# Kernel optimization log

Hardware: AMD Instinct MI355X
Metric: run time of the kernel (lower is better)

## Reference

```python
import jax, jax.numpy as jnp
import numpy as np

B, N, M, E, H = 8, 4096, 4, 512, 8
HEAD_DIM = E // H
LN_EPS = 1e-5


def setup_inputs() -> dict:
    key = jax.random.key(0)
    ks = jax.random.split(key, 12)
    inp = {}
    for i in range(M):
        inp[f"f{i}"] = jax.random.normal(ks[i], (B, N, E), dtype=jnp.float32)
    # learned query (flattened from [1,1,E])
    inp["q_param"] = jax.random.normal(ks[4], (E,), dtype=jnp.float32)
    # torch nn.MultiheadAttention packed in-projection [3E, E] and bias [3E]
    inp["in_proj_w"] = jax.random.normal(ks[5], (3 * E, E), dtype=jnp.float32) * 0.02
    inp["in_proj_b"] = jnp.zeros((3 * E,), dtype=jnp.float32)
    inp["out_proj_w"] = jax.random.normal(ks[6], (E, E), dtype=jnp.float32) * 0.02
    inp["out_proj_b"] = jnp.zeros((E,), dtype=jnp.float32)
    inp["ln_gamma"] = jnp.ones((E,), dtype=jnp.float32)
    inp["ln_beta"] = jnp.zeros((E,), dtype=jnp.float32)
    return inp


def reference(f0, f1, f2, f3, q_param, in_proj_w, in_proj_b, out_proj_w, out_proj_b, ln_gamma, ln_beta):
    x = jnp.stack([f0, f1, f2, f3], axis=2)  # [B, N, M, E]
    b, n, m, e = x.shape
    h, d = H, e // H
    scale = 1.0 / np.sqrt(d)

    Wq, Wk, Wv = jnp.split(in_proj_w, 3, axis=0)  # each [E, E]
    bq, bk, bv = jnp.split(in_proj_b, 3)

    # single learned query, shared across all (b, n) instances
    qh = ((Wq @ q_param + bq) * scale).reshape(h, d)  # [H, d]

    k = (jnp.einsum('bnme,fe->bnmf', x, Wk) + bk).reshape(b, n, m, h, d)
    v = (jnp.einsum('bnme,fe->bnmf', x, Wv) + bv).reshape(b, n, m, h, d)

    scores = jnp.einsum('hd,bnmhd->bnhm', qh, k)        # [B, N, H, M]
    attn = jax.nn.softmax(scores, axis=-1)
    o = jnp.einsum('bnhm,bnmhd->bnhd', attn, v).reshape(b, n, e)
    o = o @ out_proj_w.T + out_proj_b                   # [B, N, E]

    mu = jnp.mean(o, axis=-1, keepdims=True)
    var = jnp.var(o, axis=-1, keepdims=True)
    return (o - mu) * jax.lax.rsqrt(var + LN_EPS) * ln_gamma + ln_beta
```

## Files before the change

### kernel.cpp

```cpp
#include <hip/hip_runtime.h>
#include <hip/hip_bf16.h>


typedef float  f32x4  __attribute__((ext_vector_type(4)));
typedef float  f32x16 __attribute__((ext_vector_type(16)));
typedef short  short8 __attribute__((ext_vector_type(8)));

__device__ __forceinline__ unsigned short f2bf(float f) {
  unsigned int x = __float_as_uint(f);
  unsigned int r = (x + 0x7fffu + ((x >> 16) & 1u)) >> 16;
  return (unsigned short)r;
}

__device__ __forceinline__ short8 pack8(const f32x4& a, const f32x4& b) {
  short8 r;
  r[0] = (short)f2bf(a[0]); r[1] = (short)f2bf(a[1]);
  r[2] = (short)f2bf(a[2]); r[3] = (short)f2bf(a[3]);
  r[4] = (short)f2bf(b[0]); r[5] = (short)f2bf(b[1]);
  r[6] = (short)f2bf(b[2]); r[7] = (short)f2bf(b[3]);
  return r;
}

__device__ __forceinline__ void mfma32(f32x16& c, short8 a, short8 b) {
  asm("v_mfma_f32_32x32x16_bf16 %0, %1, %2, %0" : "+v"(c) : "v"(a), "v"(b));
}
__device__ __forceinline__ void mfma16(f32x4& c, short8 a, short8 b) {
  asm("v_mfma_f32_16x16x32_bf16 %0, %1, %2, %0" : "+v"(c) : "v"(a), "v"(b));
}

__device__ __forceinline__ void gld4f(f32x4& d, const float* p) {
  asm volatile("global_load_dwordx4 %0, %1, off" : "=v"(d) : "v"(p));
}
__device__ __forceinline__ void gld4s(short8& d, const unsigned short* p) {
  asm volatile("global_load_dwordx4 %0, %1, off" : "=v"(d) : "v"(p));
}

__device__ __forceinline__ void wxv4(f32x4& a, f32x4& b, f32x4& c, f32x4& d) {
  asm volatile("s_waitcnt vmcnt(4)" : "+v"(a), "+v"(b), "+v"(c), "+v"(d));
}
__device__ __forceinline__ void wxv8(f32x4& a, f32x4& b, f32x4& c, f32x4& d) {
  asm volatile("s_waitcnt vmcnt(8)" : "+v"(a), "+v"(b), "+v"(c), "+v"(d));
}
__device__ __forceinline__ void wxv12(f32x4& a, f32x4& b, f32x4& c, f32x4& d) {
  asm volatile("s_waitcnt vmcnt(12)" : "+v"(a), "+v"(b), "+v"(c), "+v"(d));
}
__device__ __forceinline__ void wbv4(short8& a, short8& b, short8& c, short8& d,
                                     short8& e, short8& f, short8& g, short8& h) {
  asm volatile("s_waitcnt vmcnt(4)"
               : "+v"(a), "+v"(b), "+v"(c), "+v"(d),
                 "+v"(e), "+v"(f), "+v"(g), "+v"(h));
}
__device__ __forceinline__ void wbv0(short8& a, short8& b, short8& c, short8& d,
                                     short8& e, short8& f, short8& g, short8& h) {
  asm volatile("s_waitcnt vmcnt(0)"
               : "+v"(a), "+v"(b), "+v"(c), "+v"(d),
                 "+v"(e), "+v"(f), "+v"(g), "+v"(h));
}

__global__ void __launch_bounds__(512) tdcp_k0(
    const float* __restrict__ q_param, const float* __restrict__ in_w,
    const float* __restrict__ in_b, const float* __restrict__ out_w,
    float* __restrict__ scoreb, unsigned short* __restrict__ wscB,
    unsigned short* __restrict__ WvB, unsigned short* __restrict__ WoB)
{
  const int tid = threadIdx.x;
  const int blk = blockIdx.x;
  if (blk < 8) {
    const int h = blk;
    __shared__ float qls[512];
    __shared__ float qs[64];
    qls[tid] = q_param[tid];
    __syncthreads();
    {
      const int io = tid >> 3, sub = tid & 7;
      const float* wrow = in_w + (size_t)(h * 64 + io) * 512;
      float v = 0.f;
      #pragma unroll 8
      for (int ee = 0; ee < 64; ++ee) {
        const int e = sub + (ee << 3);
        v += wrow[e] * qls[e];
      }
      v += __shfl_xor(v, 1); v += __shfl_xor(v, 2); v += __shfl_xor(v, 4);
      if (sub == 0) qs[io] = (v + in_b[h * 64 + io]) * 0.125f;
    }
    __syncthreads();
    {
      const int e = tid;
      const float* wk = in_w + (size_t)(512 + h * 64) * 512 + e;
      float v = 0.f;
      #pragma unroll 8
      for (int jj = 0; jj < 64; ++jj) v += qs[jj] * wk[jj * 512];
      const int s32 = e >> 5, g = (e & 31) >> 3, j = e & 7;
      wscB[((s32 << 6) + h + (g << 4)) * 8 + j] = f2bf(v);
      wscB[((s32 << 6) + (h + 8) + (g << 4)) * 8 + j] = 0;
    }
    if (tid < 64) {
      float v = qs[tid] * in_b[512 + h * 64 + tid];
      v += __shfl_xor(v, 1);  v += __shfl_xor(v, 2);  v += __shfl_xor(v, 4);
      v += __shfl_xor(v, 8);  v += __shfl_xor(v, 16); v += __shfl_xor(v, 32);
      if (tid == 0) scoreb[h] = v;
    }
    if (blk == 0 && tid >= 64 && tid < 72) scoreb[tid - 56] = 0.f;
  } else {
    const int mb = blk - 8;
    const bool isWo = mb >= 64;
    const float* src = isWo ? out_w : (in_w + (size_t)1024 * 512);
    unsigned short* dst = isWo ? WoB : WvB;
    const int slot = ((mb & 63) << 9) + tid;
    const int ct = slot >> 11, kt = (slot >> 6) & 31, ln = slot & 63;
    const float* p = src + (size_t)(ct * 32 + (ln & 31)) * 512
                         + kt * 16 + ((ln >> 5) << 3);
    const f32x4 u0 = *(const f32x4*)(p);
    const f32x4 u1 = *(const f32x4*)(p + 4);
    *(short8*)(dst + slot * 8) = pack8(u0, u1);
  }
}

__global__ void __launch_bounds__(512, 2) tdcp_k1(
    const float* __restrict__ f0, const float* __restrict__ f1,
    const float* __restrict__ f2, const float* __restrict__ f3,
    const float* __restrict__ in_b,
    const float* __restrict__ scoreb, const unsigned short* __restrict__ wscB,
    const unsigned short* __restrict__ WvB, const unsigned short* __restrict__ WoB,
    const float* __restrict__ out_b, const float* __restrict__ gamma,
    const float* __restrict__ beta, float* __restrict__ out)
{
  __shared__ __align__(16) char smem[65536];
  const int tid = threadIdx.x;
  const int w = tid >> 6;
  const int l = tid & 63;
  const int tok0 = blockIdx.x << 5;

  {
    const f32x4* wsrc = (const f32x4*)wscB;
    f32x4* wdst = (f32x4*)(smem + 49152);
    wdst[tid * 2] = wsrc[tid * 2];
    wdst[tid * 2 + 1] = wsrc[tid * 2 + 1];
  }

  const int sr = tid >> 2;
  const int chunk = tid & 3;
  const int sm = sr & 3;
  const int stk = sr >> 2;
  const float* fsrc = (sm == 0 ? f0 : sm == 1 ? f1 : sm == 2 ? f2 : f3)
                      + (size_t)(tok0 + stk) * 512 + (chunk << 4);
  const int wbase = (chunk << 12) + ((sr >> 5) << 10)
                  + (((sr & 31) << 4) ^ (chunk << 5));

  const int aO = ((l >> 5) << 9) + ((l & 31) << 4);
  const int sBase = ((w >> 1) << 10) + (((l >> 4) & 1) << 9)
                  + ((((w & 1) << 4) | (l & 15)) << 4);
  const int ct0 = w << 1;
  const unsigned short* wv0 = WvB + (((ct0 * 32) << 6) + l) * 8;
  const unsigned short* wv1 = WvB + ((((ct0 + 1) * 32) << 6) + l) * 8;
  const unsigned short* wscL = (const unsigned short*)(smem + 49152);

  f32x16 acc[4][2];
  f32x4 sacc;
  #pragma unroll
  for (int i = 0; i < 4; ++i)
    #pragma unroll
    for (int c = 0; c < 2; ++c)
      #pragma unroll
      for (int r = 0; r < 16; ++r) acc[i][c][r] = 0.f;
  sacc[0] = sacc[1] = sacc[2] = sacc[3] = 0.f;

  f32x4 lx[2][4];
  short8 bb[2][8];

  gld4f(lx[0][0], fsrc);      gld4f(lx[0][1], fsrc + 4);
  gld4f(lx[0][2], fsrc + 8);  gld4f(lx[0][3], fsrc + 12);
  gld4f(lx[1][0], fsrc + 64); gld4f(lx[1][1], fsrc + 68);
  gld4f(lx[1][2], fsrc + 72); gld4f(lx[1][3], fsrc + 76);
  wxv4(lx[0][0], lx[0][1], lx[0][2], lx[0][3]);
  *(short8*)(smem + wbase) = pack8(lx[0][0], lx[0][1]);
  *(short8*)(smem + wbase + 512) = pack8(lx[0][2], lx[0][3]);
  #pragma unroll
  for (int j = 0; j < 4; ++j) {
    gld4s(bb[0][2 * j],     wv0 + j * 512);
    gld4s(bb[0][2 * j + 1], wv1 + j * 512);
  }
  gld4f(lx[0][0], fsrc + 128); gld4f(lx[0][1], fsrc + 132);
  gld4f(lx[0][2], fsrc + 136); gld4f(lx[0][3], fsrc + 140);
  asm volatile("s_waitcnt lgkmcnt(0)" ::: "memory");
  __builtin_amdgcn_s_barrier();
  asm volatile("" ::: "memory");

  #pragma unroll
  for (int s = 0; s < 8; ++s) {
    if (s < 7) {
      f32x4 (&L)[4] = lx[(s + 1) & 1];
      if (s < 6) wxv12(L[0], L[1], L[2], L[3]);
      else       wxv8(L[0], L[1], L[2], L[3]);
      char* nb = smem + 16384 * ((s + 1) % 3);
      *(short8*)(nb + wbase) = pack8(L[0], L[1]);
      *(short8*)(nb + wbase + 512) = pack8(L[2], L[3]);
    }
    asm volatile("s_waitcnt lgkmcnt(0)" ::: "memory");
    __builtin_amdgcn_s_barrier();
    asm volatile("" ::: "memory");

    short8 (&b)[8] = bb[s & 1];
    if (s < 6) wbv4(b[0], b[1], b[2], b[3], b[4], b[5], b[6], b[7]);
    else       wbv0(b[0], b[1], b[2], b[3], b[4], b[5], b[6], b[7]);
    char* cur = smem + 16384 * (s % 3);
    const short8 sb0 = *(const short8*)(wscL + (((2 * s) << 6) + l) * 8);
    const short8 sb1 = *(const short8*)(wscL + (((2 * s + 1) << 6) + l) * 8);
    #pragma unroll
    for (int kt4 = 0; kt4 < 4; ++kt4) {
      #pragma unroll
      for (int rt = 0; rt < 4; ++rt) {
        const short8 a = *(const short8*)(cur + (kt4 << 12) + (rt << 10)
                                          + (aO ^ (kt4 << 5)));
        mfma32(acc[rt][0], a, b[kt4 * 2]);
        mfma32(acc[rt][1], a, b[kt4 * 2 + 1]);
      }
      if ((kt4 & 1) == 0) {
        const int schunk = kt4 + (l >> 5);
        const short8 sa = *(const short8*)(cur + (schunk << 12)
                                           + (sBase ^ ((schunk & 3) << 5)));
        mfma16(sacc, sa, (kt4 == 0) ? sb0 : sb1);
      }
    }
    if (s < 7) {
      short8 (&nbf)[8] = bb[(s + 1) & 1];
      #pragma unroll
      for (int j = 0; j < 4; ++j) {
        gld4s(nbf[2 * j],     wv0 + ((s + 1) * 4 + j) * 512);
        gld4s(nbf[2 * j + 1], wv1 + ((s + 1) * 4 + j) * 512);
      }
    }
    if (s < 5) {
      f32x4 (&L)[4] = lx[(s + 3) & 1];
      const float* p = fsrc + ((s + 3) << 6);
      gld4f(L[0], p); gld4f(L[1], p + 4); gld4f(L[2], p + 8); gld4f(L[3], p + 12);
    }
  }
  asm volatile("s_nop 7\n\ts_nop 7\n\ts_nop 7" ::);

  {
    const int hh = l & 15;
    if (hh < 8) {
      const float sb = scoreb[hh];
      const float s0 = sacc[0] + sb, s1 = sacc[1] + sb;
      const float s2 = sacc[2] + sb, s3 = sacc[3] + sb;
      const float mx = fmaxf(fmaxf(s0, s1), fmaxf(s2, s3));
      const float e0 = __expf(s0 - mx), e1 = __expf(s1 - mx);
      const float e2 = __expf(s2 - mx), e3 = __expf(s3 - mx);
      const float inv = 1.f / (e0 + e1 + e2 + e3);
      f32x4 av; av[0] = e0 * inv; av[1] = e1 * inv; av[2] = e2 * inv; av[3] = e3 * inv;
      const int t = (w << 2) + (l >> 4);
      *(f32x4*)(smem + 32768 + (((t << 3) + hh) << 4)) = av;
    }
  }
  __syncthreads();

  {
    unsigned short* omid = (unsigned short*)(smem);
    #pragma unroll
    for (int c2 = 0; c2 < 2; ++c2) {
      const int ff = ((ct0 + c2) << 5) + (l & 31);
      const float bvf = in_b[1024 + ff];
      const int ktf = ff >> 4;
      const int laneL = ((l >> 3) & 1) << 5;
      const int elem = ff & 7;
      #pragma unroll
      for (int rt = 0; rt < 4; ++rt) {
        #pragma unroll
        for (int tt = 0; tt < 4; ++tt) {
          const int t = (rt << 3) + (tt << 1) + (l >> 5);
          const f32x4 av = *(const f32x4*)(smem + 32768 + (((t << 3) + w) << 4));
          const float o = av[0] * acc[rt][c2][tt * 4 + 0]
                        + av[1] * acc[rt][c2][tt * 4 + 1]
                        + av[2] * acc[rt][c2][tt * 4 + 2]
                        + av[3] * acc[rt][c2][tt * 4 + 3] + bvf;
          omid[((ktf << 6) + t + laneL) * 8 + elem] = f2bf(o);
        }
      }
    }
  }
  __syncthreads();

  f32x16 oa0, oa1;
  #pragma unroll
  for (int r = 0; r < 16; ++r) { oa0[r] = 0.f; oa1[r] = 0.f; }
  const int a_off = l << 4;
  #pragma unroll 4
  for (int kt = 0; kt < 32; ++kt) {
    const short8 a = *(const short8*)(smem + (kt << 10) + a_off);
    const short8 b0 = *(const short8*)(WoB + (((ct0 * 32 + kt) << 6) + l) * 8);
    const short8 b1 = *(const short8*)(WoB + ((((ct0 + 1) * 32 + kt) << 6) + l) * 8);
    mfma32(oa0, a, b0);
    mfma32(oa1, a, b1);
  }
  asm volatile("s_nop 7\n\ts_nop 7\n\ts_nop 7" ::);

  {
    const int g0 = (ct0 << 5) + (l & 31);
    const int g1 = g0 + 32;
    const float ob0 = out_b[g0], ob1 = out_b[g1];
    const float gm0 = gamma[g0], gm1 = gamma[g1];
    const float bt0 = beta[g0],  bt1 = beta[g1];
    float* stats = (float*)(smem + 36864);
    #pragma unroll
    for (int r = 0; r < 16; ++r) {
      const float v0 = oa0[r] + ob0, v1 = oa1[r] + ob1;
      float s = v0 + v1, qq = v0 * v0 + v1 * v1;
      s += __shfl_xor(s, 16); qq += __shfl_xor(qq, 16);
      s += __shfl_xor(s, 8);  qq += __shfl_xor(qq, 8);
      s += __shfl_xor(s, 4);  qq += __shfl_xor(qq, 4);
      s += __shfl_xor(s, 2);  qq += __shfl_xor(qq, 2);
      s += __shfl_xor(s, 1);  qq += __shfl_xor(qq, 1);
      if ((l & 31) == 0) {
        const int t = (r & 3) + ((r >> 2) << 3) + ((l >> 5) << 2);
        stats[(t << 4) + (w << 1)] = s;
        stats[(t << 4) + (w << 1) + 1] = qq;
      }
    }
    __syncthreads();
    #pragma unroll
    for (int r = 0; r < 16; ++r) {
      const int t = (r & 3) + ((r >> 2) << 3) + ((l >> 5) << 2);
      const float* st = stats + (t << 4);
      float s = 0.f, qq = 0.f;
      #pragma unroll
      for (int ww = 0; ww < 8; ++ww) { s += st[2 * ww]; qq += st[2 * ww + 1]; }
      const float mu = s * 0.001953125f;
      const float rs = rsqrtf(qq * 0.001953125f - mu * mu + 1e-5f);
      const float v0 = oa0[r] + ob0, v1 = oa1[r] + ob1;
      float* op = out + (size_t)(tok0 + t) * 512;
      op[g0] = (v0 - mu) * rs * gm0 + bt0;
      op[g1] = (v1 - mu) * rs * gm1 + bt1;
    }
  }
}

extern "C" void kernel_launch(void* const* d_in, const int* in_sizes, int n_in,
                              void* d_out, int out_size, void* d_ws, size_t ws_size,
                              hipStream_t stream) {
  const float* f0      = (const float*)d_in[0];
  const float* f1      = (const float*)d_in[1];
  const float* f2      = (const float*)d_in[2];
  const float* f3      = (const float*)d_in[3];
  const float* q_param = (const float*)d_in[4];
  const float* in_w    = (const float*)d_in[5];
  const float* in_b    = (const float*)d_in[6];
  const float* out_w   = (const float*)d_in[7];
  const float* out_b   = (const float*)d_in[8];
  const float* gamma   = (const float*)d_in[9];
  const float* beta    = (const float*)d_in[10];
  float* out = (float*)d_out;

  char* ws = (char*)d_ws;
  float* scoreb          = (float*)ws;
  unsigned short* wscB   = (unsigned short*)(ws + 4096);
  unsigned short* WvB    = (unsigned short*)(ws + 20480);
  unsigned short* WoB    = (unsigned short*)(ws + 544768);

  tdcp_k0<<<136, 512, 0, stream>>>(q_param, in_w, in_b, out_w,
                                   scoreb, wscB, WvB, WoB);
  tdcp_k1<<<1024, 512, 0, stream>>>(f0, f1, f2, f3, in_b,
                                    scoreb, wscB, WvB, WoB,
                                    out_b, gamma, beta, out);
}
```

Before: 152.6 us.

## Double block size to 16 waves, one output column tile per wave

The fused attention/out-projection kernel now runs 1024 threads per block instead of 512. Each wave owns a single 32-column tile of the V projection and of the output projection instead of two, which halves its accumulators, prefetched weight fragments and staged input registers. Staging loads, waitcnt depths and the LayerNorm statistics layout are resized to fit 16 waves, and only the first 8 waves compute the attention scores. Separately, bf16 packing now uses the hardware v_cvt_pk_bf16_f32 instruction instead of software rounding. The aim is to hide memory latency with more waves in flight; the risk is that the aggressive launch bounds squeeze registers too hard, and barriers across 16 waves cost more.

```diff
diff --git a/kernel.cpp b/kernel.cpp
--- a/kernel.cpp
+++ b/kernel.cpp
@@ -13,11 +13,16 @@
 }
 
 __device__ __forceinline__ short8 pack8(const f32x4& a, const f32x4& b) {
+  unsigned int r0, r1, r2, r3;
+  asm("v_cvt_pk_bf16_f32 %0, %1, %2" : "=v"(r0) : "v"(a[0]), "v"(a[1]));
+  asm("v_cvt_pk_bf16_f32 %0, %1, %2" : "=v"(r1) : "v"(a[2]), "v"(a[3]));
+  asm("v_cvt_pk_bf16_f32 %0, %1, %2" : "=v"(r2) : "v"(b[0]), "v"(b[1]));
+  asm("v_cvt_pk_bf16_f32 %0, %1, %2" : "=v"(r3) : "v"(b[2]), "v"(b[3]));
   short8 r;
-  r[0] = (short)f2bf(a[0]); r[1] = (short)f2bf(a[1]);
-  r[2] = (short)f2bf(a[2]); r[3] = (short)f2bf(a[3]);
-  r[4] = (short)f2bf(b[0]); r[5] = (short)f2bf(b[1]);
-  r[6] = (short)f2bf(b[2]); r[7] = (short)f2bf(b[3]);
+  r[0] = (short)(r0 & 0xffff); r[1] = (short)(r0 >> 16);
+  r[2] = (short)(r1 & 0xffff); r[3] = (short)(r1 >> 16);
+  r[4] = (short)(r2 & 0xffff); r[5] = (short)(r2 >> 16);
+  r[6] = (short)(r3 & 0xffff); r[7] = (short)(r3 >> 16);
   return r;
 }
 
@@ -35,26 +40,20 @@
   asm volatile("global_load_dwordx4 %0, %1, off" : "=v"(d) : "v"(p));
 }
 
-__device__ __forceinline__ void wxv4(f32x4& a, f32x4& b, f32x4& c, f32x4& d) {
-  asm volatile("s_waitcnt vmcnt(4)" : "+v"(a), "+v"(b), "+v"(c), "+v"(d));
-}
-__device__ __forceinline__ void wxv8(f32x4& a, f32x4& b, f32x4& c, f32x4& d) {
-  asm volatile("s_waitcnt vmcnt(8)" : "+v"(a), "+v"(b), "+v"(c), "+v"(d));
-}
-__device__ __forceinline__ void wxv12(f32x4& a, f32x4& b, f32x4& c, f32x4& d) {
-  asm volatile("s_waitcnt vmcnt(12)" : "+v"(a), "+v"(b), "+v"(c), "+v"(d));
-}
-__device__ __forceinline__ void wbv4(short8& a, short8& b, short8& c, short8& d,
-                                     short8& e, short8& f, short8& g, short8& h) {
-  asm volatile("s_waitcnt vmcnt(4)"
-               : "+v"(a), "+v"(b), "+v"(c), "+v"(d),
-                 "+v"(e), "+v"(f), "+v"(g), "+v"(h));
-}
-__device__ __forceinline__ void wbv0(short8& a, short8& b, short8& c, short8& d,
-                                     short8& e, short8& f, short8& g, short8& h) {
-  asm volatile("s_waitcnt vmcnt(0)"
-               : "+v"(a), "+v"(b), "+v"(c), "+v"(d),
-                 "+v"(e), "+v"(f), "+v"(g), "+v"(h));
+__device__ __forceinline__ void wxv2(f32x4& a, f32x4& b) {
+  asm volatile("s_waitcnt vmcnt(2)" : "+v"(a), "+v"(b));
+}
+__device__ __forceinline__ void wxv4(f32x4& a, f32x4& b) {
+  asm volatile("s_waitcnt vmcnt(4)" : "+v"(a), "+v"(b));
+}
+__device__ __forceinline__ void wxv6(f32x4& a, f32x4& b) {
+  asm volatile("s_waitcnt vmcnt(6)" : "+v"(a), "+v"(b));
+}
+__device__ __forceinline__ void wbv2(short8& a, short8& b, short8& c, short8& d) {
+  asm volatile("s_waitcnt vmcnt(2)" : "+v"(a), "+v"(b), "+v"(c), "+v"(d));
+}
+__device__ __forceinline__ void wbv0(short8& a, short8& b, short8& c, short8& d) {
+  asm volatile("s_waitcnt vmcnt(0)" : "+v"(a), "+v"(b), "+v"(c), "+v"(d));
 }
 
 __global__ void __launch_bounds__(512) tdcp_k0(
@@ -112,11 +111,18 @@
                          + kt * 16 + ((ln >> 5) << 3);
     const f32x4 u0 = *(const f32x4*)(p);
     const f32x4 u1 = *(const f32x4*)(p + 4);
-    *(short8*)(dst + slot * 8) = pack8(u0, u1);
-  }
-}
-
-__global__ void __launch_bounds__(512, 2) tdcp_k1(
+    unsigned int r0, r1, r2, r3;
+    short8 rr;
+    rr[0] = (short)f2bf(u0[0]); rr[1] = (short)f2bf(u0[1]);
+    rr[2] = (short)f2bf(u0[2]); rr[3] = (short)f2bf(u0[3]);
+    rr[4] = (short)f2bf(u1[0]); rr[5] = (short)f2bf(u1[1]);
+    rr[6] = (short)f2bf(u1[2]); rr[7] = (short)f2bf(u1[3]);
+    *(short8*)(dst + slot * 8) = rr;
+    (void)r0; (void)r1; (void)r2; (void)r3;
+  }
+}
+
+__global__ void __launch_bounds__(1024, 4) tdcp_k1(
     const float* __restrict__ f0, const float* __restrict__ f1,
     const float* __restrict__ f2, const float* __restrict__ f3,
     const float* __restrict__ in_b,
@@ -134,54 +140,44 @@
   {
     const f32x4* wsrc = (const f32x4*)wscB;
     f32x4* wdst = (f32x4*)(smem + 49152);
-    wdst[tid * 2] = wsrc[tid * 2];
-    wdst[tid * 2 + 1] = wsrc[tid * 2 + 1];
-  }
-
-  const int sr = tid >> 2;
-  const int chunk = tid & 3;
+    wdst[tid] = wsrc[tid];
+  }
+
+  const int sr = tid >> 3;
+  const int c16 = (tid & 7) >> 1;
+  const int half = tid & 1;
   const int sm = sr & 3;
   const int stk = sr >> 2;
   const float* fsrc = (sm == 0 ? f0 : sm == 1 ? f1 : sm == 2 ? f2 : f3)
-                      + (size_t)(tok0 + stk) * 512 + (chunk << 4);
-  const int wbase = (chunk << 12) + ((sr >> 5) << 10)
-                  + (((sr & 31) << 4) ^ (chunk << 5));
+                      + (size_t)(tok0 + stk) * 512 + ((tid & 7) << 3);
+  const int wbase = (c16 << 12) + ((sr >> 5) << 10)
+                  + (((sr & 31) << 4) ^ (c16 << 5)) + (half << 9);
 
   const int aO = ((l >> 5) << 9) + ((l & 31) << 4);
   const int sBase = ((w >> 1) << 10) + (((l >> 4) & 1) << 9)
                   + ((((w & 1) << 4) | (l & 15)) << 4);
-  const int ct0 = w << 1;
-  const unsigned short* wv0 = WvB + (((ct0 * 32) << 6) + l) * 8;
-  const unsigned short* wv1 = WvB + ((((ct0 + 1) * 32) << 6) + l) * 8;
+  const unsigned short* wv = WvB + (((w * 32) << 6) + l) * 8;
+  const unsigned short* wo = WoB + (((w * 32) << 6) + l) * 8;
   const unsigned short* wscL = (const unsigned short*)(smem + 49152);
 
-  f32x16 acc[4][2];
+  f32x16 acc[4];
   f32x4 sacc;
   #pragma unroll
   for (int i = 0; i < 4; ++i)
     #pragma unroll
-    for (int c = 0; c < 2; ++c)
-      #pragma unroll
-      for (int r = 0; r < 16; ++r) acc[i][c][r] = 0.f;
+    for (int r = 0; r < 16; ++r) acc[i][r] = 0.f;
   sacc[0] = sacc[1] = sacc[2] = sacc[3] = 0.f;
 
-  f32x4 lx[2][4];
-  short8 bb[2][8];
+  f32x4 lx[2][2];
+  short8 bb[4];
 
   gld4f(lx[0][0], fsrc);      gld4f(lx[0][1], fsrc + 4);
-  gld4f(lx[0][2], fsrc + 8);  gld4f(lx[0][3], fsrc + 12);
   gld4f(lx[1][0], fsrc + 64); gld4f(lx[1][1], fsrc + 68);
-  gld4f(lx[1][2], fsrc + 72); gld4f(lx[1][3], fsrc + 76);
-  wxv4(lx[0][0], lx[0][1], lx[0][2], lx[0][3]);
+  wxv2(lx[0][0], lx[0][1]);
   *(short8*)(smem + wbase) = pack8(lx[0][0], lx[0][1]);
-  *(short8*)(smem + wbase + 512) = pack8(lx[0][2], lx[0][3]);
   #pragma unroll
-  for (int j = 0; j < 4; ++j) {
-    gld4s(bb[0][2 * j],     wv0 + j * 512);
-    gld4s(bb[0][2 * j + 1], wv1 + j * 512);
-  }
+  for (int j = 0; j < 4; ++j) gld4s(bb[j], wv + j * 512);
   gld4f(lx[0][0], fsrc + 128); gld4f(lx[0][1], fsrc + 132);
-  gld4f(lx[0][2], fsrc + 136); gld4f(lx[0][3], fsrc + 140);
   asm volatile("s_waitcnt lgkmcnt(0)" ::: "memory");
   __builtin_amdgcn_s_barrier();
   asm volatile("" ::: "memory");
@@ -189,56 +185,50 @@
   #pragma unroll
   for (int s = 0; s < 8; ++s) {
     if (s < 7) {
-      f32x4 (&L)[4] = lx[(s + 1) & 1];
-      if (s < 6) wxv12(L[0], L[1], L[2], L[3]);
-      else       wxv8(L[0], L[1], L[2], L[3]);
+      f32x4 (&L)[2] = lx[(s + 1) & 1];
+      if (s < 6) wxv6(L[0], L[1]);
+      else       wxv4(L[0], L[1]);
       char* nb = smem + 16384 * ((s + 1) % 3);
       *(short8*)(nb + wbase) = pack8(L[0], L[1]);
-      *(short8*)(nb + wbase + 512) = pack8(L[2], L[3]);
     }
     asm volatile("s_waitcnt lgkmcnt(0)" ::: "memory");
     __builtin_amdgcn_s_barrier();
     asm volatile("" ::: "memory");
 
-    short8 (&b)[8] = bb[s & 1];
-    if (s < 6) wbv4(b[0], b[1], b[2], b[3], b[4], b[5], b[6], b[7]);
-    else       wbv0(b[0], b[1], b[2], b[3], b[4], b[5], b[6], b[7]);
+    if (s < 6) wbv2(bb[0], bb[1], bb[2], bb[3]);
+    else       wbv0(bb[0], bb[1], bb[2], bb[3]);
     char* cur = smem + 16384 * (s % 3);
-    const short8 sb0 = *(const short8*)(wscL + (((2 * s) << 6) + l) * 8);
-    const short8 sb1 = *(const short8*)(wscL + (((2 * s + 1) << 6) + l) * 8);
     #pragma unroll
     for (int kt4 = 0; kt4 < 4; ++kt4) {
       #pragma unroll
       for (int rt = 0; rt < 4; ++rt) {
         const short8 a = *(const short8*)(cur + (kt4 << 12) + (rt << 10)
                                           + (aO ^ (kt4 << 5)));
-        mfma32(acc[rt][0], a, b[kt4 * 2]);
-        mfma32(acc[rt][1], a, b[kt4 * 2 + 1]);
-      }
-      if ((kt4 & 1) == 0) {
+        mfma32(acc[rt], a, bb[kt4]);
+      }
+      if (w < 8 && (kt4 & 1) == 0) {
         const int schunk = kt4 + (l >> 5);
         const short8 sa = *(const short8*)(cur + (schunk << 12)
                                            + (sBase ^ ((schunk & 3) << 5)));
-        mfma16(sacc, sa, (kt4 == 0) ? sb0 : sb1);
+        const short8 sb = *(const short8*)(wscL
+                            + (((2 * s + (kt4 >> 1)) << 6) + l) * 8);
+        mfma16(sacc, sa, sb);
       }
     }
     if (s < 7) {
-      short8 (&nbf)[8] = bb[(s + 1) & 1];
       #pragma unroll
-      for (int j = 0; j < 4; ++j) {
-        gld4s(nbf[2 * j],     wv0 + ((s + 1) * 4 + j) * 512);
-        gld4s(nbf[2 * j + 1], wv1 + ((s + 1) * 4 + j) * 512);
-      }
+      for (int j = 0; j < 4; ++j)
+        gld4s(bb[j], wv + ((s + 1) * 4 + j) * 512);
     }
     if (s < 5) {
-      f32x4 (&L)[4] = lx[(s + 3) & 1];
+      f32x4 (&L)[2] = lx[(s + 3) & 1];
       const float* p = fsrc + ((s + 3) << 6);
-      gld4f(L[0], p); gld4f(L[1], p + 4); gld4f(L[2], p + 8); gld4f(L[3], p + 12);
+      gld4f(L[0], p); gld4f(L[1], p + 4);
     }
   }
   asm volatile("s_nop 7\n\ts_nop 7\n\ts_nop 7" ::);
 
-  {
+  if (w < 8) {
     const int hh = l & 15;
     if (hh < 8) {
       const float sb = scoreb[hh];
@@ -257,55 +247,50 @@
 
   {
     unsigned short* omid = (unsigned short*)(smem);
-    #pragma unroll
-    for (int c2 = 0; c2 < 2; ++c2) {
-      const int ff = ((ct0 + c2) << 5) + (l & 31);
-      const float bvf = in_b[1024 + ff];
-      const int ktf = ff >> 4;
-      const int laneL = ((l >> 3) & 1) << 5;
-      const int elem = ff & 7;
+    const int ff = (w << 5) + (l & 31);
+    const float bvf = in_b[1024 + ff];
+    const int ktf = ff >> 4;
+    const int laneL = ((l >> 3) & 1) << 5;
+    const int elem = ff & 7;
+    const int hq = w >> 1;
+    #pragma unroll
+    for (int rt = 0; rt < 4; ++rt) {
       #pragma unroll
-      for (int rt = 0; rt < 4; ++rt) {
-        #pragma unroll
-        for (int tt = 0; tt < 4; ++tt) {
-          const int t = (rt << 3) + (tt << 1) + (l >> 5);
-          const f32x4 av = *(const f32x4*)(smem + 32768 + (((t << 3) + w) << 4));
-          const float o = av[0] * acc[rt][c2][tt * 4 + 0]
-                        + av[1] * acc[rt][c2][tt * 4 + 1]
-                        + av[2] * acc[rt][c2][tt * 4 + 2]
-                        + av[3] * acc[rt][c2][tt * 4 + 3] + bvf;
-          omid[((ktf << 6) + t + laneL) * 8 + elem] = f2bf(o);
-        }
+      for (int tt = 0; tt < 4; ++tt) {
+        const int t = (rt << 3) + (tt << 1) + (l >> 5);
+        const f32x4 av = *(const f32x4*)(smem + 32768 + (((t << 3) + hq) << 4));
+        const float o = av[0] * acc[rt][tt * 4 + 0]
+                      + av[1] * acc[rt][tt * 4 + 1]
+                      + av[2] * acc[rt][tt * 4 + 2]
+                      + av[3] * acc[rt][tt * 4 + 3] + bvf;
+        omid[((ktf << 6) + t + laneL) * 8 + elem] = f2bf(o);
       }
     }
   }
   __syncthreads();
 
-  f32x16 oa0, oa1;
+  f32x16 oa;
   #pragma unroll
-  for (int r = 0; r < 16; ++r) { oa0[r] = 0.f; oa1[r] = 0.f; }
+  for (int r = 0; r < 16; ++r) oa[r] = 0.f;
   const int a_off = l << 4;
   #pragma unroll 4
   for (int kt = 0; kt < 32; ++kt) {
     const short8 a = *(const short8*)(smem + (kt << 10) + a_off);
-    const short8 b0 = *(const short8*)(WoB + (((ct0 * 32 + kt) << 6) + l) * 8);
-    const short8 b1 = *(const short8*)(WoB + ((((ct0 + 1) * 32 + kt) << 6) + l) * 8);
-    mfma32(oa0, a, b0);
-    mfma32(oa1, a, b1);
+    const short8 b0 = *(const short8*)(wo + kt * 512);
+    mfma32(oa, a, b0);
   }
   asm volatile("s_nop 7\n\ts_nop 7\n\ts_nop 7" ::);
 
   {
-    const int g0 = (ct0 << 5) + (l & 31);
-    const int g1 = g0 + 32;
-    const float ob0 = out_b[g0], ob1 = out_b[g1];
-    const float gm0 = gamma[g0], gm1 = gamma[g1];
-    const float bt0 = beta[g0],  bt1 = beta[g1];
+    const int g0 = (w << 5) + (l & 31);
+    const float ob0 = out_b[g0];
+    const float gm0 = gamma[g0];
+    const float bt0 = beta[g0];
     float* stats = (float*)(smem + 36864);
     #pragma unroll
     for (int r = 0; r < 16; ++r) {
-      const float v0 = oa0[r] + ob0, v1 = oa1[r] + ob1;
-      float s = v0 + v1, qq = v0 * v0 + v1 * v1;
+      const float v0 = oa[r] + ob0;
+      float s = v0, qq = v0 * v0;
       s += __shfl_xor(s, 16); qq += __shfl_xor(qq, 16);
       s += __shfl_xor(s, 8);  qq += __shfl_xor(qq, 8);
       s += __shfl_xor(s, 4);  qq += __shfl_xor(qq, 4);
@@ -313,24 +298,25 @@
       s += __shfl_xor(s, 1);  qq += __shfl_xor(qq, 1);
       if ((l & 31) == 0) {
         const int t = (r & 3) + ((r >> 2) << 3) + ((l >> 5) << 2);
-        stats[(t << 4) + (w << 1)] = s;
-        stats[(t << 4) + (w << 1) + 1] = qq;
+        stats[(t << 5) + (w << 1)] = s;
+        stats[(t << 5) + (w << 1) + 1] = qq;
       }
     }
     __syncthreads();
     #pragma unroll
     for (int r = 0; r < 16; ++r) {
       const int t = (r & 3) + ((r >> 2) << 3) + ((l >> 5) << 2);
-      const float* st = stats + (t << 4);
+      const float* st = (const float*)(smem + 36864) + (t << 5);
       float s = 0.f, qq = 0.f;
       #pragma unroll
-      for (int ww = 0; ww < 8; ++ww) { s += st[2 * ww]; qq += st[2 * ww + 1]; }
+      for (int ww = 0; ww < 8; ++ww) {
+        const f32x4 u = *(const f32x4*)(st + (ww << 2));
+        s += u[0] + u[2]; qq += u[1] + u[3];
+      }
       const float mu = s * 0.001953125f;
       const float rs = rsqrtf(qq * 0.001953125f - mu * mu + 1e-5f);
-      const float v0 = oa0[r] + ob0, v1 = oa1[r] + ob1;
-      float* op = out + (size_t)(tok0 + t) * 512;
-      op[g0] = (v0 - mu) * rs * gm0 + bt0;
-      op[g1] = (v1 - mu) * rs * gm1 + bt1;
+      const float v0 = oa[r] + ob0;
+      out[(size_t)(tok0 + t) * 512 + g0] = (v0 - mu) * rs * gm0 + bt0;
     }
   }
 }
@@ -359,7 +345,7 @@
 
   tdcp_k0<<<136, 512, 0, stream>>>(q_param, in_w, in_b, out_w,
                                    scoreb, wscB, WvB, WoB);
-  tdcp_k1<<<1024, 512, 0, stream>>>(f0, f1, f2, f3, in_b,
-                                    scoreb, wscB, WvB, WoB,
-                                    out_b, gamma, beta, out);
-}
+  tdcp_k1<<<1024, 1024, 0, stream>>>(f0, f1, f2, f3, in_b,
+                                     scoreb, wscB, WvB, WoB,
+                                     out_b, gamma, beta, out);
+}
```

Result: slower. 170.7 us (+11.8%).

## Use hardware bf16 pack conversion and interleave x-tile loads to strided 4-float chunks

Applied to the files above, without the earlier changes.

Replaces the software round-to-nearest bf16 conversion in the hot activation path with the v_cvt_pk_bf16_f32 instruction, keeping the software path only in the weight prep kernel. Changes how each thread loads its x slice, from 16 contiguous floats to four 4-float chunks strided by 16, and writes them as four 8-byte LDS stores at recomputed swizzled offsets. This aims to cut VALU conversion cost and improve global load coalescing across lanes. Also hoists the Wo pointer arithmetic out of the output GEMM loop. The new LDS layout must match the MFMA read pattern exactly, and the narrower stores could raise LDS store count or bank conflicts.

```diff
diff --git a/kernel.cpp b/kernel.cpp
--- a/kernel.cpp
+++ b/kernel.cpp
@@ -5,6 +5,7 @@
 typedef float  f32x4  __attribute__((ext_vector_type(4)));
 typedef float  f32x16 __attribute__((ext_vector_type(16)));
 typedef short  short8 __attribute__((ext_vector_type(8)));
+typedef unsigned int u32x2 __attribute__((ext_vector_type(2)));
 
 __device__ __forceinline__ unsigned short f2bf(float f) {
   unsigned int x = __float_as_uint(f);
@@ -13,11 +14,23 @@
 }
 
 __device__ __forceinline__ short8 pack8(const f32x4& a, const f32x4& b) {
+  unsigned int r0, r1, r2, r3;
+  asm("v_cvt_pk_bf16_f32 %0, %1, %2" : "=v"(r0) : "v"(a[0]), "v"(a[1]));
+  asm("v_cvt_pk_bf16_f32 %0, %1, %2" : "=v"(r1) : "v"(a[2]), "v"(a[3]));
+  asm("v_cvt_pk_bf16_f32 %0, %1, %2" : "=v"(r2) : "v"(b[0]), "v"(b[1]));
+  asm("v_cvt_pk_bf16_f32 %0, %1, %2" : "=v"(r3) : "v"(b[2]), "v"(b[3]));
   short8 r;
-  r[0] = (short)f2bf(a[0]); r[1] = (short)f2bf(a[1]);
-  r[2] = (short)f2bf(a[2]); r[3] = (short)f2bf(a[3]);
-  r[4] = (short)f2bf(b[0]); r[5] = (short)f2bf(b[1]);
-  r[6] = (short)f2bf(b[2]); r[7] = (short)f2bf(b[3]);
+  r[0] = (short)(r0 & 0xffff); r[1] = (short)(r0 >> 16);
+  r[2] = (short)(r1 & 0xffff); r[3] = (short)(r1 >> 16);
+  r[4] = (short)(r2 & 0xffff); r[5] = (short)(r2 >> 16);
+  r[6] = (short)(r3 & 0xffff); r[7] = (short)(r3 >> 16);
+  return r;
+}
+
+__device__ __forceinline__ u32x2 pack4(const f32x4& a) {
+  u32x2 r;
+  asm("v_cvt_pk_bf16_f32 %0, %1, %2" : "=v"(r[0]) : "v"(a[0]), "v"(a[1]));
+  asm("v_cvt_pk_bf16_f32 %0, %1, %2" : "=v"(r[1]) : "v"(a[2]), "v"(a[3]));
   return r;
 }
 
@@ -112,7 +125,12 @@
                          + kt * 16 + ((ln >> 5) << 3);
     const f32x4 u0 = *(const f32x4*)(p);
     const f32x4 u1 = *(const f32x4*)(p + 4);
-    *(short8*)(dst + slot * 8) = pack8(u0, u1);
+    short8 rr;
+    rr[0] = (short)f2bf(u0[0]); rr[1] = (short)f2bf(u0[1]);
+    rr[2] = (short)f2bf(u0[2]); rr[3] = (short)f2bf(u0[3]);
+    rr[4] = (short)f2bf(u1[0]); rr[5] = (short)f2bf(u1[1]);
+    rr[6] = (short)f2bf(u1[2]); rr[7] = (short)f2bf(u1[3]);
+    *(short8*)(dst + slot * 8) = rr;
   }
 }
 
@@ -139,13 +157,16 @@
   }
 
   const int sr = tid >> 2;
-  const int chunk = tid & 3;
+  const int c = tid & 3;
   const int sm = sr & 3;
   const int stk = sr >> 2;
   const float* fsrc = (sm == 0 ? f0 : sm == 1 ? f1 : sm == 2 ? f2 : f3)
-                      + (size_t)(tok0 + stk) * 512 + (chunk << 4);
-  const int wbase = (chunk << 12) + ((sr >> 5) << 10)
-                  + (((sr & 31) << 4) ^ (chunk << 5));
+                      + (size_t)(tok0 + stk) * 512 + (c << 2);
+  int wj[4];
+  #pragma unroll
+  for (int j = 0; j < 4; ++j)
+    wj[j] = (j << 12) + ((sr >> 5) << 10) + ((c >> 1) << 9)
+          + ((((sr & 31) << 4)) ^ (j << 5)) + ((c & 1) << 3);
 
   const int aO = ((l >> 5) << 9) + ((l & 31) << 4);
   const int sBase = ((w >> 1) << 10) + (((l >> 4) & 1) << 9)
@@ -160,28 +181,29 @@
   #pragma unroll
   for (int i = 0; i < 4; ++i)
     #pragma unroll
-    for (int c = 0; c < 2; ++c)
-      #pragma unroll
-      for (int r = 0; r < 16; ++r) acc[i][c][r] = 0.f;
+    for (int cc = 0; cc < 2; ++cc)
+      #pragma unroll
+      for (int r = 0; r < 16; ++r) acc[i][cc][r] = 0.f;
   sacc[0] = sacc[1] = sacc[2] = sacc[3] = 0.f;
 
   f32x4 lx[2][4];
   short8 bb[2][8];
 
-  gld4f(lx[0][0], fsrc);      gld4f(lx[0][1], fsrc + 4);
-  gld4f(lx[0][2], fsrc + 8);  gld4f(lx[0][3], fsrc + 12);
-  gld4f(lx[1][0], fsrc + 64); gld4f(lx[1][1], fsrc + 68);
-  gld4f(lx[1][2], fsrc + 72); gld4f(lx[1][3], fsrc + 76);
+  gld4f(lx[0][0], fsrc);      gld4f(lx[0][1], fsrc + 16);
+  gld4f(lx[0][2], fsrc + 32); gld4f(lx[0][3], fsrc + 48);
+  gld4f(lx[1][0], fsrc + 64); gld4f(lx[1][1], fsrc + 80);
+  gld4f(lx[1][2], fsrc + 96); gld4f(lx[1][3], fsrc + 112);
   wxv4(lx[0][0], lx[0][1], lx[0][2], lx[0][3]);
-  *(short8*)(smem + wbase) = pack8(lx[0][0], lx[0][1]);
-  *(short8*)(smem + wbase + 512) = pack8(lx[0][2], lx[0][3]);
+  #pragma unroll
+  for (int j = 0; j < 4; ++j)
+    *(u32x2*)(smem + wj[j]) = pack4(lx[0][j]);
   #pragma unroll
   for (int j = 0; j < 4; ++j) {
     gld4s(bb[0][2 * j],     wv0 + j * 512);
     gld4s(bb[0][2 * j + 1], wv1 + j * 512);
   }
-  gld4f(lx[0][0], fsrc + 128); gld4f(lx[0][1], fsrc + 132);
-  gld4f(lx[0][2], fsrc + 136); gld4f(lx[0][3], fsrc + 140);
+  gld4f(lx[0][0], fsrc + 128); gld4f(lx[0][1], fsrc + 144);
+  gld4f(lx[0][2], fsrc + 160); gld4f(lx[0][3], fsrc + 176);
   asm volatile("s_waitcnt lgkmcnt(0)" ::: "memory");
   __builtin_amdgcn_s_barrier();
   asm volatile("" ::: "memory");
@@ -193,8 +215,9 @@
       if (s < 6) wxv12(L[0], L[1], L[2], L[3]);
       else       wxv8(L[0], L[1], L[2], L[3]);
       char* nb = smem + 16384 * ((s + 1) % 3);
-      *(short8*)(nb + wbase) = pack8(L[0], L[1]);
-      *(short8*)(nb + wbase + 512) = pack8(L[2], L[3]);
+      #pragma unroll
+      for (int j = 0; j < 4; ++j)
+        *(u32x2*)(nb + wj[j]) = pack4(L[j]);
     }
     asm volatile("s_waitcnt lgkmcnt(0)" ::: "memory");
     __builtin_amdgcn_s_barrier();
@@ -233,7 +256,7 @@
     if (s < 5) {
       f32x4 (&L)[4] = lx[(s + 3) & 1];
       const float* p = fsrc + ((s + 3) << 6);
-      gld4f(L[0], p); gld4f(L[1], p + 4); gld4f(L[2], p + 8); gld4f(L[3], p + 12);
+      gld4f(L[0], p); gld4f(L[1], p + 16); gld4f(L[2], p + 32); gld4f(L[3], p + 48);
     }
   }
   asm volatile("s_nop 7\n\ts_nop 7\n\ts_nop 7" ::);
@@ -284,14 +307,14 @@
   f32x16 oa0, oa1;
   #pragma unroll
   for (int r = 0; r < 16; ++r) { oa0[r] = 0.f; oa1[r] = 0.f; }
+  const unsigned short* wo0 = WoB + (((ct0 * 32) << 6) + l) * 8;
+  const unsigned short* wo1 = WoB + ((((ct0 + 1) * 32) << 6) + l) * 8;
   const int a_off = l << 4;
   #pragma unroll 4
   for (int kt = 0; kt < 32; ++kt) {
     const short8 a = *(const short8*)(smem + (kt << 10) + a_off);
-    const short8 b0 = *(const short8*)(WoB + (((ct0 * 32 + kt) << 6) + l) * 8);
-    const short8 b1 = *(const short8*)(WoB + ((((ct0 + 1) * 32 + kt) << 6) + l) * 8);
-    mfma32(oa0, a, b0);
-    mfma32(oa1, a, b1);
+    mfma32(oa0, a, *(const short8*)(wo0 + kt * 512));
+    mfma32(oa1, a, *(const short8*)(wo1 + kt * 512));
   }
   asm volatile("s_nop 7\n\ts_nop 7\n\ts_nop 7" ::);
 
```

Result: faster. 149.0 us, median of 2 (-2.4%).
